# Performance work log

Hardware: AMD Instinct MI355X
Metric: run time of the kernel (lower is better)

The kernel has to match this reference:

```python
import jax, jax.numpy as jnp
import numpy as np

B, T, IN, H, OUT = 512, 1000, 39, 64, 48


def setup_inputs() -> dict:
    key = jax.random.key(0)
    ks = jax.random.split(key, 7)
    s = 1.0 / np.sqrt(H)
    return {
        "x": jax.random.normal(ks[0], (B, T, IN), dtype=jnp.float32),
        "W_ih": jax.random.uniform(ks[1], (4 * H, IN), minval=-s, maxval=s, dtype=jnp.float32),
        "W_hh": jax.random.uniform(ks[2], (4 * H, H), minval=-s, maxval=s, dtype=jnp.float32),
        "b_ih": jax.random.uniform(ks[3], (4 * H,), minval=-s, maxval=s, dtype=jnp.float32),
        "b_hh": jax.random.uniform(ks[4], (4 * H,), minval=-s, maxval=s, dtype=jnp.float32),
        "W_out": jax.random.uniform(ks[5], (OUT, H), minval=-s, maxval=s, dtype=jnp.float32),
        "b_out": jax.random.uniform(ks[6], (OUT,), minval=-s, maxval=s, dtype=jnp.float32),
    }


def reference(x, W_ih, W_hh, b_ih, b_hh, W_out, b_out):
    # Single-layer batch-first LSTM (zero init state) + per-step Linear + sigmoid.
    b = b_ih + b_hh  # [4H]
    # Precompute input projections for all timesteps at once: [T, B, 4H]
    xg = jnp.einsum('bti,gi->tbg', x, W_ih) + b

    def step(carry, xg_t):
        h, c = carry
        gates = xg_t + h @ W_hh.T  # [B, 4H], gate order i, f, g, o
        i, f, g, o = jnp.split(gates, 4, axis=-1)
        c = jax.nn.sigmoid(f) * c + jax.nn.sigmoid(i) * jnp.tanh(g)
        h = jax.nn.sigmoid(o) * jnp.tanh(c)
        y = jax.nn.sigmoid(h @ W_out.T + b_out)  # [B, OUT]
        return (h, c), y

    h0 = jnp.zeros((x.shape[0], W_hh.shape[1]), dtype=x.dtype)
    (_, _), ys = jax.lax.scan(step, (h0, h0), xg)  # ys: [T, B, OUT]
    return jnp.swapaxes(ys, 0, 1)  # [B, T, OUT]
```

## Files before the change

### kernel.cpp

```cpp
#include <hip/hip_runtime.h>


#define BB 512
#define TT 1000
#define INF 39
#define HH 64
#define OUTF 48
#define G4 (4 * HH)

#define Q10(M) M(0) M(1) M(2) M(3) M(4) M(5) M(6) M(7) M(8) M(9)
#define Q16(M) M(0) M(1) M(2) M(3) M(4) M(5) M(6) M(7) \
               M(8) M(9) M(10) M(11) M(12) M(13) M(14) M(15)

__global__ __launch_bounds__(256, 2) void lstm_fused_kernel(
    const float* __restrict__ x,
    const float* __restrict__ W_ih,
    const float* __restrict__ W_hh,
    const float* __restrict__ b_ih,
    const float* __restrict__ b_hh,
    const float* __restrict__ W_out,
    const float* __restrict__ b_out,
    float* __restrict__ out)
{
    const int b = blockIdx.x;
    const int tid = threadIdx.x;

    __shared__ float xs[40];
    __shared__ float hs[HH];
    __shared__ float act[G4];

    const float* wih_ptr = W_ih + tid * INF;
#define LOAD_IH4(q) float4 wiq##q; \
    wiq##q.x = wih_ptr[4*(q)]; \
    wiq##q.y = (4*(q)+1 < INF) ? wih_ptr[4*(q)+1] : 0.f; \
    wiq##q.z = (4*(q)+2 < INF) ? wih_ptr[4*(q)+2] : 0.f; \
    wiq##q.w = (4*(q)+3 < INF) ? wih_ptr[4*(q)+3] : 0.f;
    Q10(LOAD_IH4)

    const float4* wh4p = (const float4*)(W_hh + tid * HH);
#define LOAD_HH4(i) const float4 wh##i = wh4p[i];
    Q16(LOAD_HH4)

    const float bias = b_ih[tid] + b_hh[tid];

    const int o = tid >> 2;
    const int p = tid & 3;
    float4 wo0, wo1, wo2, wo3;
    float bo = 0.f;
    if (tid < 4 * OUTF) {
        const float4* wop = (const float4*)(W_out + o * HH + p * 16);
        wo0 = wop[0]; wo1 = wop[1]; wo2 = wop[2]; wo3 = wop[3];
        bo = b_out[o];
    } else {
        wo0 = wo1 = wo2 = wo3 = make_float4(0.f, 0.f, 0.f, 0.f);
    }

    float c = 0.f;
    const size_t x_base = (size_t)b * TT * INF;
    const size_t out_base = (size_t)b * TT * OUTF;

    if (tid < HH) hs[tid] = 0.f;
    if (tid < INF) xs[tid] = x[x_base + tid];
    if (tid == 39) xs[39] = 0.f;
    float xreg = (tid < INF) ? x[x_base + INF + tid] : 0.f;

    const int gate_type = tid >> 6;
    __syncthreads();

    const float4* xs4 = (const float4*)xs;
    const float4* hs4 = (const float4*)hs;

    for (int t = 0; t < TT; ++t) {
        float a0 = bias, a1 = 0.f, a2 = 0.f, a3 = 0.f;
#define FMA_IH4(q) { const float4 xv = xs4[q]; \
        a0 += xv.x * wiq##q.x; a1 += xv.y * wiq##q.y; \
        a2 += xv.z * wiq##q.z; a3 += xv.w * wiq##q.w; }
        Q10(FMA_IH4)
#define FMA_HH4(i) { const float4 hv = hs4[i]; \
        a0 += hv.x * wh##i.x; a1 += hv.y * wh##i.y; \
        a2 += hv.z * wh##i.z; a3 += hv.w * wh##i.w; }
        Q16(FMA_HH4)
        const float acc = (a0 + a1) + (a2 + a3);

        float a;
        if (gate_type == 2) {
            a = 2.f / (1.f + __expf(-2.f * acc)) - 1.f;
        } else {
            a = 1.f / (1.f + __expf(-acc));
        }
        act[tid] = a;
        __syncthreads();

        if (tid < INF) {
            xs[tid] = xreg;
            if (t + 2 < TT) xreg = x[x_base + (size_t)(t + 2) * INF + tid];
        }
        if (tid < HH) {
            const float ig = act[tid];
            const float fg = act[HH + tid];
            const float gg = act[2 * HH + tid];
            const float og = act[3 * HH + tid];
            c = fg * c + ig * gg;
            const float th = 2.f / (1.f + __expf(-2.f * c)) - 1.f;
            hs[tid] = og * th;
        }
        __syncthreads();

        if (tid < 4 * OUTF) {
            const float4 h0 = hs4[p * 4 + 0];
            const float4 h1 = hs4[p * 4 + 1];
            const float4 h2 = hs4[p * 4 + 2];
            const float4 h3 = hs4[p * 4 + 3];
            float s0 = h0.x * wo0.x + h0.y * wo0.y + h0.z * wo0.z + h0.w * wo0.w;
            float s1 = h1.x * wo1.x + h1.y * wo1.y + h1.z * wo1.z + h1.w * wo1.w;
            float s2 = h2.x * wo2.x + h2.y * wo2.y + h2.z * wo2.z + h2.w * wo2.w;
            float s3 = h3.x * wo3.x + h3.y * wo3.y + h3.z * wo3.z + h3.w * wo3.w;
            float s = (s0 + s1) + (s2 + s3);
            s += __shfl_xor(s, 1, 64);
            s += __shfl_xor(s, 2, 64);
            if (p == 0) {
                const float y = 1.f / (1.f + __expf(-(s + bo)));
                __builtin_nontemporal_store(y, &out[out_base + (size_t)t * OUTF + o]);
            }
        }
    }
}

extern "C" void kernel_launch(void* const* d_in, const int* in_sizes, int n_in,
                              void* d_out, int out_size, void* d_ws, size_t ws_size,
                              hipStream_t stream) {
    const float* x     = (const float*)d_in[0];
    const float* W_ih  = (const float*)d_in[1];
    const float* W_hh  = (const float*)d_in[2];
    const float* b_ih  = (const float*)d_in[3];
    const float* b_hh  = (const float*)d_in[4];
    const float* W_out = (const float*)d_in[5];
    const float* b_out = (const float*)d_in[6];
    float* out = (float*)d_out;

    lstm_fused_kernel<<<dim3(BB), dim3(G4), 0, stream>>>(
        x, W_ih, W_hh, b_ih, b_hh, W_out, b_out, out);
}
```

Measured before the change: 1.076 ms.

## Split LSTM gate dots over K across waves and defer output projection a step

Changes the work split: each wave now computes partial sums over a 16-wide slice of h and a 10-wide slice of x for all four gates of one hidden unit. Wave 0 reduces the partials through shared memory and applies the cell update, and the output projection for step t-1 is computed from the same h loads, overlapping it with step t. Adds double-buffered h and x buffers and packed float2 FMAs, and drops to one block per CU in the launch bounds. The intent is to remove one barrier per step and the serialized output phase, at the cost of more shared-memory traffic for the partial reductions and fewer resident blocks.

New measurement: 879.3 us. -18.3%, faster.

```diff
diff --git a/kernel.cpp b/kernel.cpp
--- a/kernel.cpp
+++ b/kernel.cpp
@@ -6,122 +6,166 @@
 #define INF 39
 #define HH 64
 #define OUTF 48
-#define G4 (4 * HH)
 
-#define Q10(M) M(0) M(1) M(2) M(3) M(4) M(5) M(6) M(7) M(8) M(9)
-#define Q16(M) M(0) M(1) M(2) M(3) M(4) M(5) M(6) M(7) \
-               M(8) M(9) M(10) M(11) M(12) M(13) M(14) M(15)
+typedef float v2f __attribute__((ext_vector_type(2)));
 
-__global__ __launch_bounds__(256, 2) void lstm_fused_kernel(
-    const float* __restrict__ x,
-    const float* __restrict__ W_ih,
-    const float* __restrict__ W_hh,
-    const float* __restrict__ b_ih,
-    const float* __restrict__ b_hh,
-    const float* __restrict__ W_out,
-    const float* __restrict__ b_out,
-    float* __restrict__ out)
+__device__ __forceinline__ float sigf(float v)  { return 1.f / (1.f + __expf(-v)); }
+__device__ __forceinline__ float tanhx(float v) { return 2.f / (1.f + __expf(-2.f * v)) - 1.f; }
+
+#define Q5(M, G)  M(G,0) M(G,1) M(G,2) M(G,3) M(G,4)
+#define Q8(M, G)  M(G,0) M(G,1) M(G,2) M(G,3) M(G,4) M(G,5) M(G,6) M(G,7)
+
+__global__ __launch_bounds__(256, 1)
+void lstm_regw(const float* __restrict__ x,
+               const float* __restrict__ W_ih,
+               const float* __restrict__ W_hh,
+               const float* __restrict__ b_ih,
+               const float* __restrict__ b_hh,
+               const float* __restrict__ W_out,
+               const float* __restrict__ b_out,
+               float* __restrict__ out)
 {
-    const int b = blockIdx.x;
     const int tid = threadIdx.x;
+    const int j   = tid & 63;
+    const int w   = tid >> 6;
+    const int b   = blockIdx.x;
 
-    __shared__ float xs[40];
-    __shared__ float hs[HH];
-    __shared__ float act[G4];
+    __shared__ __align__(16) float  hsb[2][HH];
+    __shared__ __align__(16) float  xsb[2][48];
+    __shared__ __align__(16) float4 parts[4][64];
+    __shared__ float                 yp[4][64];
 
-    const float* wih_ptr = W_ih + tid * INF;
-#define LOAD_IH4(q) float4 wiq##q; \
-    wiq##q.x = wih_ptr[4*(q)]; \
-    wiq##q.y = (4*(q)+1 < INF) ? wih_ptr[4*(q)+1] : 0.f; \
-    wiq##q.z = (4*(q)+2 < INF) ? wih_ptr[4*(q)+2] : 0.f; \
-    wiq##q.w = (4*(q)+3 < INF) ? wih_ptr[4*(q)+3] : 0.f;
-    Q10(LOAD_IH4)
+    const size_t xb = (size_t)b * TT * INF;
+    const size_t ob = (size_t)b * TT * OUTF;
 
-    const float4* wh4p = (const float4*)(W_hh + tid * HH);
-#define LOAD_HH4(i) const float4 wh##i = wh4p[i];
-    Q16(LOAD_HH4)
+#define LHH(g, q) v2f whh##g##_##q; { \
+    const v2f* p_ = (const v2f*)(W_hh + ((g)*HH + j) * HH + 16 * w); \
+    whh##g##_##q = p_[q]; } \
+    asm volatile("" : "+v"(whh##g##_##q));
+    Q8(LHH, 0) Q8(LHH, 1) Q8(LHH, 2) Q8(LHH, 3)
 
-    const float bias = b_ih[tid] + b_hh[tid];
+#define LIH(g, q) v2f wih##g##_##q; { \
+    const float* p_ = W_ih + ((g)*HH + j) * INF + 10 * w; \
+    wih##g##_##q.x = (10*w + 2*(q)     < INF) ? p_[2*(q)]     : 0.f; \
+    wih##g##_##q.y = (10*w + 2*(q) + 1 < INF) ? p_[2*(q) + 1] : 0.f; } \
+    asm volatile("" : "+v"(wih##g##_##q));
+    Q5(LIH, 0) Q5(LIH, 1) Q5(LIH, 2) Q5(LIH, 3)
 
-    const int o = tid >> 2;
-    const int p = tid & 3;
-    float4 wo0, wo1, wo2, wo3;
-    float bo = 0.f;
-    if (tid < 4 * OUTF) {
-        const float4* wop = (const float4*)(W_out + o * HH + p * 16);
-        wo0 = wop[0]; wo1 = wop[1]; wo2 = wop[2]; wo3 = wop[3];
-        bo = b_out[o];
-    } else {
-        wo0 = wo1 = wo2 = wo3 = make_float4(0.f, 0.f, 0.f, 0.f);
+#define LWO(g, q) v2f wo_##q;
+#define LWO2(dummy, q) v2f wo_##q = {0.f, 0.f}; \
+    if (j < OUTF) { \
+        const v2f* p_ = (const v2f*)(W_out + j * HH + 16 * w); \
+        wo_##q = p_[q]; } \
+    asm volatile("" : "+v"(wo_##q));
+    Q8(LWO2, 0)
+
+    const float bg0 = b_ih[0*HH+j] + b_hh[0*HH+j];
+    const float bg1 = b_ih[1*HH+j] + b_hh[1*HH+j];
+    const float bg2 = b_ih[2*HH+j] + b_hh[2*HH+j];
+    const float bg3 = b_ih[3*HH+j] + b_hh[3*HH+j];
+    const float bo  = (j < OUTF) ? b_out[j] : 0.f;
+
+    if (tid < 96)  ((float*)xsb)[tid] = 0.f;
+    if (tid >= 128) ((float*)hsb)[tid - 128] = 0.f;
+    __syncthreads();
+    float xreg = 0.f;
+    if (w == 2 && j < INF) {
+        xsb[0][(j / 10) * 12 + (j % 10)] = x[xb + j];
+        xreg = x[xb + INF + j];
+    }
+    float c = 0.f;
+    __syncthreads();
+
+    for (int t = 0; t < TT; ++t) {
+        const int par = t & 1;
+        const float4* h4 = (const float4*)(hsb[par ^ 1] + 16 * w);
+        const float4 hq0 = h4[0], hq1 = h4[1], hq2 = h4[2], hq3 = h4[3];
+        const float4* x4 = (const float4*)(xsb[par] + 12 * w);
+        const float4 xq0 = x4[0], xq1 = x4[1];
+        const float2 xq2 = *(const float2*)(xsb[par] + 12 * w + 8);
+
+        float sg0, sg1, sg2, sg3;
+#define GDOT(g, OUTV) { \
+        v2f aA = {0.f, 0.f}, aB = {0.f, 0.f}; \
+        aA += (v2f){hq0.x, hq0.y} * whh##g##_0; \
+        aB += (v2f){hq0.z, hq0.w} * whh##g##_1; \
+        aA += (v2f){hq1.x, hq1.y} * whh##g##_2; \
+        aB += (v2f){hq1.z, hq1.w} * whh##g##_3; \
+        aA += (v2f){hq2.x, hq2.y} * whh##g##_4; \
+        aB += (v2f){hq2.z, hq2.w} * whh##g##_5; \
+        aA += (v2f){hq3.x, hq3.y} * whh##g##_6; \
+        aB += (v2f){hq3.z, hq3.w} * whh##g##_7; \
+        aA += (v2f){xq0.x, xq0.y} * wih##g##_0; \
+        aB += (v2f){xq0.z, xq0.w} * wih##g##_1; \
+        aA += (v2f){xq1.x, xq1.y} * wih##g##_2; \
+        aB += (v2f){xq1.z, xq1.w} * wih##g##_3; \
+        aA += (v2f){xq2.x, xq2.y} * wih##g##_4; \
+        OUTV = (aA.x + aA.y) + (aB.x + aB.y); }
+        GDOT(0, sg0) GDOT(1, sg1) GDOT(2, sg2) GDOT(3, sg3)
+#undef GDOT
+
+        float yv;
+        {
+            v2f yA = {0.f, 0.f}, yB = {0.f, 0.f};
+            yA += (v2f){hq0.x, hq0.y} * wo_0;
+            yB += (v2f){hq0.z, hq0.w} * wo_1;
+            yA += (v2f){hq1.x, hq1.y} * wo_2;
+            yB += (v2f){hq1.z, hq1.w} * wo_3;
+            yA += (v2f){hq2.x, hq2.y} * wo_4;
+            yB += (v2f){hq2.z, hq2.w} * wo_5;
+            yA += (v2f){hq3.x, hq3.y} * wo_6;
+            yB += (v2f){hq3.z, hq3.w} * wo_7;
+            yv = (yA.x + yA.y) + (yB.x + yB.y);
+        }
+
+        if (w != 0) parts[w][j] = make_float4(sg0, sg1, sg2, sg3);
+        if (w != 1) yp[w][j] = yv;
+        __syncthreads();
+
+        if (w == 0) {
+            const float4 p1 = parts[1][j];
+            const float4 p2 = parts[2][j];
+            const float4 p3 = parts[3][j];
+            const float gi = sg0 + p1.x + p2.x + p3.x + bg0;
+            const float gf = sg1 + p1.y + p2.y + p3.y + bg1;
+            const float gg = sg2 + p1.z + p2.z + p3.z + bg2;
+            const float go = sg3 + p1.w + p2.w + p3.w + bg3;
+            c = fmaf(sigf(gf), c, sigf(gi) * tanhx(gg));
+            hsb[par][j] = sigf(go) * tanhx(c);
+        } else if (w == 1) {
+            if (t >= 1 && j < OUTF) {
+                const float s = yv + yp[0][j] + yp[2][j] + yp[3][j] + bo;
+                __builtin_nontemporal_store(sigf(s),
+                    &out[ob + (size_t)(t - 1) * OUTF + j]);
+            }
+        } else if (w == 2) {
+            if (j < INF) {
+                xsb[par ^ 1][(j / 10) * 12 + (j % 10)] = xreg;
+                if (t + 2 < TT) xreg = x[xb + (size_t)(t + 2) * INF + j];
+            }
+        }
+        __syncthreads();
     }
 
-    float c = 0.f;
-    const size_t x_base = (size_t)b * TT * INF;
-    const size_t out_base = (size_t)b * TT * OUTF;
-
-    if (tid < HH) hs[tid] = 0.f;
-    if (tid < INF) xs[tid] = x[x_base + tid];
-    if (tid == 39) xs[39] = 0.f;
-    float xreg = (tid < INF) ? x[x_base + INF + tid] : 0.f;
-
-    const int gate_type = tid >> 6;
-    __syncthreads();
-
-    const float4* xs4 = (const float4*)xs;
-    const float4* hs4 = (const float4*)hs;
-
-    for (int t = 0; t < TT; ++t) {
-        float a0 = bias, a1 = 0.f, a2 = 0.f, a3 = 0.f;
-#define FMA_IH4(q) { const float4 xv = xs4[q]; \
-        a0 += xv.x * wiq##q.x; a1 += xv.y * wiq##q.y; \
-        a2 += xv.z * wiq##q.z; a3 += xv.w * wiq##q.w; }
-        Q10(FMA_IH4)
-#define FMA_HH4(i) { const float4 hv = hs4[i]; \
-        a0 += hv.x * wh##i.x; a1 += hv.y * wh##i.y; \
-        a2 += hv.z * wh##i.z; a3 += hv.w * wh##i.w; }
-        Q16(FMA_HH4)
-        const float acc = (a0 + a1) + (a2 + a3);
-
-        float a;
-        if (gate_type == 2) {
-            a = 2.f / (1.f + __expf(-2.f * acc)) - 1.f;
-        } else {
-            a = 1.f / (1.f + __expf(-acc));
-        }
-        act[tid] = a;
+    {
+        const float4* h4 = (const float4*)(hsb[1] + 16 * w);
+        const float4 hq0 = h4[0], hq1 = h4[1], hq2 = h4[2], hq3 = h4[3];
+        v2f yA = {0.f, 0.f}, yB = {0.f, 0.f};
+        yA += (v2f){hq0.x, hq0.y} * wo_0;
+        yB += (v2f){hq0.z, hq0.w} * wo_1;
+        yA += (v2f){hq1.x, hq1.y} * wo_2;
+        yB += (v2f){hq1.z, hq1.w} * wo_3;
+        yA += (v2f){hq2.x, hq2.y} * wo_4;
+        yB += (v2f){hq2.z, hq2.w} * wo_5;
+        yA += (v2f){hq3.x, hq3.y} * wo_6;
+        yB += (v2f){hq3.z, hq3.w} * wo_7;
+        const float yv = (yA.x + yA.y) + (yB.x + yB.y);
+        if (w != 1) yp[w][j] = yv;
         __syncthreads();
-
-        if (tid < INF) {
-            xs[tid] = xreg;
-            if (t + 2 < TT) xreg = x[x_base + (size_t)(t + 2) * INF + tid];
-        }
-        if (tid < HH) {
-            const float ig = act[tid];
-            const float fg = act[HH + tid];
-            const float gg = act[2 * HH + tid];
-            const float og = act[3 * HH + tid];
-            c = fg * c + ig * gg;
-            const float th = 2.f / (1.f + __expf(-2.f * c)) - 1.f;
-            hs[tid] = og * th;
-        }
-        __syncthreads();
-
-        if (tid < 4 * OUTF) {
-            const float4 h0 = hs4[p * 4 + 0];
-            const float4 h1 = hs4[p * 4 + 1];
-            const float4 h2 = hs4[p * 4 + 2];
-            const float4 h3 = hs4[p * 4 + 3];
-            float s0 = h0.x * wo0.x + h0.y * wo0.y + h0.z * wo0.z + h0.w * wo0.w;
-            float s1 = h1.x * wo1.x + h1.y * wo1.y + h1.z * wo1.z + h1.w * wo1.w;
-            float s2 = h2.x * wo2.x + h2.y * wo2.y + h2.z * wo2.z + h2.w * wo2.w;
-            float s3 = h3.x * wo3.x + h3.y * wo3.y + h3.z * wo3.z + h3.w * wo3.w;
-            float s = (s0 + s1) + (s2 + s3);
-            s += __shfl_xor(s, 1, 64);
-            s += __shfl_xor(s, 2, 64);
-            if (p == 0) {
-                const float y = 1.f / (1.f + __expf(-(s + bo)));
-                __builtin_nontemporal_store(y, &out[out_base + (size_t)t * OUTF + o]);
-            }
+        if (w == 1 && j < OUTF) {
+            const float s = yv + yp[0][j] + yp[2][j] + yp[3][j] + bo;
+            __builtin_nontemporal_store(sigf(s),
+                &out[ob + (size_t)(TT - 1) * OUTF + j]);
         }
     }
 }
@@ -138,6 +182,6 @@
     const float* b_out = (const float*)d_in[6];
     float* out = (float*)d_out;
 
-    lstm_fused_kernel<<<dim3(BB), dim3(G4), 0, stream>>>(
+    lstm_regw<<<dim3(BB), dim3(256), 0, stream>>>(
         x, W_ih, W_hh, b_ih, b_hh, W_out, b_out, out);
 }
```
